# Kernel optimization log

Hardware: AMD Instinct MI355X
Metric: run time of the kernel (lower is better)

## Reference

```python
import jax, jax.numpy as jnp
import numpy as np

EDGE_TYPES = 5
D = 256      # input_dim == output_dim
HID = 128    # hard-coded hidden size of agg MLPs


def setup_inputs() -> dict:
    key = jax.random.key(0)
    ks = jax.random.split(key, 8)
    B, E, N = 4, 8000, 2000
    edge_distribution = jax.random.uniform(ks[0], (B, E, EDGE_TYPES), dtype=jnp.float32)
    H = jax.random.normal(ks[1], (B, E, N), dtype=jnp.float32)
    ori = jax.random.normal(ks[2], (B, N, D), dtype=jnp.float32)
    # Stacked per-edge-type MLP params: Linear(D->128), ReLU, Linear(128->D)
    W1 = jax.random.normal(ks[3], (EDGE_TYPES, D, HID), dtype=jnp.float32) * (1.0 / np.sqrt(D))
    b1 = jax.random.normal(ks[4], (EDGE_TYPES, HID), dtype=jnp.float32) * 0.01
    W2 = jax.random.normal(ks[5], (EDGE_TYPES, HID, D), dtype=jnp.float32) * (1.0 / np.sqrt(HID))
    b2 = jax.random.normal(ks[6], (EDGE_TYPES, D), dtype=jnp.float32) * 0.01
    return {"edge_distribution": edge_distribution, "H": H, "ori": ori,
            "W1": W1, "b1": b1, "W2": W2, "b2": b2}


def reference(edge_distribution, H, ori, W1, b1, W2, b2):
    # edges = H @ ori : [B, E, D]
    edges = jnp.matmul(H, ori)
    # Per-edge-type 2-layer MLP, vectorized over the type axis t
    h = jax.nn.relu(jnp.einsum('bed,tdh->tbeh', edges, W1) + b1[:, None, None, :])  # [T,B,E,HID]
    mlp_out = jnp.einsum('tbeh,thd->tbed', h, W2) + b2[:, None, None, :]            # [T,B,E,D]
    # Gated accumulate: sum_t edge_distribution[...,t] * mlp_out[t]
    edge_feature = jnp.einsum('bet,tbed->bed', edge_distribution, mlp_out)          # [B,E,D]
    # node_feature = concat(H^T @ edge_feature, ori)
    node_feature = jnp.concatenate(
        [jnp.matmul(jnp.swapaxes(H, 1, 2), edge_feature), ori], axis=-1)            # [B,N,2D]
    return node_feature
```

## Files before the change

### kernel.cpp

```cpp
#include <hip/hip_runtime.h>
#include <hip/hip_bf16.h>

typedef unsigned short u16;
typedef short bf16x8 __attribute__((ext_vector_type(8)));
typedef float f32x4 __attribute__((ext_vector_type(4)));
typedef unsigned short u16x8 __attribute__((ext_vector_type(8)));

#define GLL16(gp, lp) __builtin_amdgcn_global_load_lds( \
    (__attribute__((address_space(1))) const unsigned int*)(gp), \
    (__attribute__((address_space(3))) unsigned int*)(lp), 16, 0, 0)

static __device__ __forceinline__ u16 f2bf(float f){
  return __builtin_bit_cast(u16, __float2bfloat16(f));
}

__global__ void transpose_f32(const float* __restrict__ src, u16* __restrict__ dst,
                              int R, int C, int Rpad, long sB, long dB){
  __shared__ u16 tile[32][33];
  const int b = blockIdx.z;
  src += (long)b*sB; dst += (long)b*dB;
  const int r0 = blockIdx.x*32, c0 = blockIdx.y*32;
  const int j = threadIdx.x & 31, i0 = threadIdx.x >> 5;
  #pragma unroll
  for (int ii=0; ii<32; ii+=8){
    int r = r0+i0+ii, c = c0+j;
    u16 v = 0;
    if (r < R && c < C) v = f2bf(src[(long)r*C + c]);
    tile[i0+ii][j] = v;
  }
  __syncthreads();
  #pragma unroll
  for (int ii=0; ii<32; ii+=8){
    int c = c0+i0+ii, r = r0+j;
    if (c < C && r < Rpad) dst[(long)c*Rpad + r] = tile[j][i0+ii];
  }
}

__global__ __launch_bounds__(512,2) void g1_kernel(
    const float* __restrict__ Hm, const u16* __restrict__ oriT,
    u16* __restrict__ edges, u16* __restrict__ HT){
  __shared__ u16 As[2][128*32];
  __shared__ u16 Bs[2][256*32];
  __shared__ u16 At[2][32*136];
  const int b = blockIdx.y, bm = blockIdx.x*128;
  const int tid = threadIdx.x;
  const int w = tid>>6, quad = (tid&63)>>4, l16 = tid&15;
  const int wm = (w&1)*64, wn = (w>>1)*64;
  const float* Ab = Hm + (size_t)b*8000*2000 + (size_t)bm*2000;
  const u16*  Bb = oriT + (size_t)b*256*2048;
  u16* HTb = HT + (size_t)b*2048*8000;
  const bool edge_blk = (bm == 7936);

  float4 pa[2];
  auto loadA = [&](int kt, bool guard){
    const int k0 = kt*32;
    #pragma unroll
    for (int i=0;i<2;i++){
      int idx = i*512+tid, row = idx>>3, c4 = (idx&7)*4;
      if (!guard){
        pa[i] = *(const float4*)(Ab + (size_t)row*2000 + k0+c4);
      } else {
        bool ok = (bm+row < 8000) && (k0+c4 < 2000);
        pa[i] = ok ? *(const float4*)(Ab + (size_t)row*2000 + k0+c4) : make_float4(0.f,0.f,0.f,0.f);
      }
    }
  };
  auto storeA = [&](int kt){
    const int buf = kt&1;
    #pragma unroll
    for (int i=0;i<2;i++){
      int idx = i*512+tid, row = idx>>3, c4 = (idx&7)*4;
      ushort4 o; o.x=f2bf(pa[i].x); o.y=f2bf(pa[i].y); o.z=f2bf(pa[i].z); o.w=f2bf(pa[i].w);
      *(ushort4*)(&As[buf][idx*4]) = o;
      At[buf][(c4+0)*136 + (row ^ ((((c4+0)>>3)&3)<<3))] = o.x;
      At[buf][(c4+1)*136 + (row ^ ((((c4+1)>>3)&3)<<3))] = o.y;
      At[buf][(c4+2)*136 + (row ^ ((((c4+2)>>3)&3)<<3))] = o.z;
      At[buf][(c4+3)*136 + (row ^ ((((c4+3)>>3)&3)<<3))] = o.w;
    }
  };
  auto stageB = [&](int kt){
    const int buf = kt&1, k0 = kt*32;
    #pragma unroll
    for (int i=0;i<2;i++){
      int idx = i*512+tid;
      int row = idx>>2, c8 = (idx&3)*8;
      GLL16(Bb + (size_t)row*2048 + k0+c8, &Bs[buf][(i*512 + w*64)*8]);
    }
  };

  f32x4 acc[4][4];
  #pragma unroll
  for (int i=0;i<4;i++)
    #pragma unroll
    for (int j=0;j<4;j++) acc[i][j] = (f32x4){0.f,0.f,0.f,0.f};

  loadA(0, edge_blk); stageB(0);
  for (int kt=0; kt<64; kt++){
    storeA(kt);
    __syncthreads();
    if (kt+1 < 64){ loadA(kt+1, edge_blk || (kt+1 >= 62)); stageB(kt+1); }
    const int buf = kt&1, k0 = kt*32;
    {
      int kk = tid>>4, c = tid&15, m0 = c*8;
      if (bm + m0 < 8000){
        u16x8 v = *(const u16x8*)(&At[buf][kk*136 + (m0 ^ (((kk>>3)&3)<<3))]);
        *(u16x8*)(HTb + (size_t)(k0+kk)*8000 + bm + m0) = v;
      }
    }
    bf16x8 af[4], bf[4];
    #pragma unroll
    for (int mi=0;mi<4;mi++) af[mi] = *(const bf16x8*)(&As[buf][(wm+mi*16+l16)*32 + quad*8]);
    #pragma unroll
    for (int ni=0;ni<4;ni++) bf[ni] = *(const bf16x8*)(&Bs[buf][(wn+ni*16+l16)*32 + quad*8]);
    #pragma unroll
    for (int mi=0;mi<4;mi++)
      #pragma unroll
      for (int ni=0;ni<4;ni++)
        acc[mi][ni] = __builtin_amdgcn_mfma_f32_16x16x32_bf16(af[mi], bf[ni], acc[mi][ni], 0,0,0);
  }
  #pragma unroll
  for (int mi=0;mi<4;mi++){
    #pragma unroll
    for (int r=0;r<4;r++){
      int gm = bm + wm + mi*16 + quad*4 + r;
      if (gm >= 8000) continue;
      u16* dst = edges + ((size_t)b*8000 + gm)*256;
      #pragma unroll
      for (int ni=0;ni<4;ni++) dst[wn + ni*16 + l16] = f2bf(acc[mi][ni][r]);
    }
  }
}

__global__ __launch_bounds__(512,2) void mlp_kernel(
    const u16* __restrict__ edges, const u16* __restrict__ W1T, const u16* __restrict__ W2T,
    const float* __restrict__ b1, const float* __restrict__ b2,
    const float* __restrict__ edist, u16* __restrict__ EFt){
  __shared__ u16 Es[8*4096];
  __shared__ u16 Hs[4*4096];
  __shared__ u16 Bs[2][256*32];
  __shared__ float eds[640], b1s[640], b2s[1280];
  const int bm = blockIdx.x*128;
  const int tid = threadIdx.x;
  const int w = tid>>6, quad = (tid&63)>>4, l16 = tid&15;
  const int wm1 = (w&1)*64, wh1 = (w>>1)*32;
  const int wd2 = (w&3)*64, wm2 = (w>>2)*64;

  for (int i=tid;i<640;i+=512){ eds[i] = edist[(size_t)bm*5 + i]; b1s[i] = b1[i]; }
  for (int i=tid;i<1280;i+=512) b2s[i] = b2[i];

  const u16* Eb = edges + (size_t)bm*256;
  {
    int row = tid>>2, c8 = (tid&3)*8;
    #pragma unroll
    for (int kt=0;kt<8;kt++)
      GLL16(Eb + (size_t)row*256 + kt*32 + c8, &Es[kt*4096 + (w*64)*8]);
  }

  auto stage1 = [&](int t, int kt){
    const int buf = kt&1;
    int row = tid>>2, c8 = (tid&3)*8;
    GLL16(W1T + ((size_t)t*128 + row)*256 + kt*32 + c8, &Bs[buf][(w*64)*8]);
  };
  auto stage2 = [&](int t, int kk){
    const int buf = kk&1;
    #pragma unroll
    for (int i=0;i<2;i++){
      int idx = i*512+tid, row = idx>>2, c8 = (idx&3)*8;
      GLL16(W2T + ((size_t)t*256 + row)*128 + kk*32 + c8, &Bs[buf][(i*512 + w*64)*8]);
    }
  };

  f32x4 acc2[4][4];
  #pragma unroll
  for (int i=0;i<4;i++)
    #pragma unroll
    for (int j=0;j<4;j++) acc2[i][j] = (f32x4){0.f,0.f,0.f,0.f};

  stage1(0,0);
  for (int t=0;t<5;t++){
    f32x4 acc1[4][2];
    #pragma unroll
    for (int i=0;i<4;i++){ acc1[i][0] = (f32x4){0.f,0.f,0.f,0.f}; acc1[i][1] = (f32x4){0.f,0.f,0.f,0.f}; }
    for (int kt=0;kt<8;kt++){
      __syncthreads();
      if (kt<7) stage1(t,kt+1); else stage2(t,0);
      const int buf = kt&1;
      bf16x8 af[4], bfr[2];
      #pragma unroll
      for (int mi=0;mi<4;mi++) af[mi] = *(const bf16x8*)(&Es[kt*4096 + (wm1+mi*16+l16)*32 + quad*8]);
      #pragma unroll
      for (int ni=0;ni<2;ni++) bfr[ni] = *(const bf16x8*)(&Bs[buf][(wh1+ni*16+l16)*32 + quad*8]);
      #pragma unroll
      for (int mi=0;mi<4;mi++)
        #pragma unroll
        for (int ni=0;ni<2;ni++)
          acc1[mi][ni] = __builtin_amdgcn_mfma_f32_16x16x32_bf16(af[mi], bfr[ni], acc1[mi][ni], 0,0,0);
    }
    __syncthreads();
    #pragma unroll
    for (int mi=0;mi<4;mi++){
      #pragma unroll
      for (int r=0;r<4;r++){
        int lrow = wm1 + mi*16 + quad*4 + r;
        float s = eds[lrow*5 + t];
        #pragma unroll
        for (int ni=0;ni<2;ni++){
          int ch = wh1 + ni*16 + l16;
          float v = fmaxf(acc1[mi][ni][r] + b1s[t*128 + ch], 0.f) * s;
          Hs[(w>>1)*4096 + lrow*32 + (ni*16 + l16)] = f2bf(v);
        }
      }
    }
    for (int kk=0;kk<4;kk++){
      __syncthreads();
      if (kk<3) stage2(t,kk+1); else if (t<4) stage1(t+1,0);
      const int buf = kk&1;
      bf16x8 af2[4], bf2[4];
      #pragma unroll
      for (int mi=0;mi<4;mi++) af2[mi] = *(const bf16x8*)(&Bs[buf][(wd2+mi*16+l16)*32 + quad*8]);
      #pragma unroll
      for (int ni=0;ni<4;ni++) bf2[ni] = *(const bf16x8*)(&Hs[kk*4096 + (wm2+ni*16+l16)*32 + quad*8]);
      #pragma unroll
      for (int mi=0;mi<4;mi++)
        #pragma unroll
        for (int ni=0;ni<4;ni++)
          acc2[mi][ni] = __builtin_amdgcn_mfma_f32_16x16x32_bf16(af2[mi], bf2[ni], acc2[mi][ni], 0,0,0);
    }
  }
  #pragma unroll
  for (int mi=0;mi<4;mi++){
    #pragma unroll
    for (int r=0;r<4;r++){
      int d = wd2 + mi*16 + quad*4 + r;
      #pragma unroll
      for (int ni=0;ni<4;ni++){
        int mc = wm2 + ni*16 + l16;
        float bias = eds[mc*5+0]*b2s[d] + eds[mc*5+1]*b2s[256+d] + eds[mc*5+2]*b2s[512+d]
                   + eds[mc*5+3]*b2s[768+d] + eds[mc*5+4]*b2s[1024+d];
        int e = bm + mc;
        int bq = e / 8000;
        EFt[((size_t)bq*256 + d)*8000 + (e - bq*8000)] = f2bf(acc2[mi][ni][r] + bias);
      }
    }
  }
}

__global__ __launch_bounds__(512,2) void g3_kernel(
    const u16* __restrict__ HT, const u16* __restrict__ EFt, float* __restrict__ part){
  __shared__ u16 As[2][128*32];
  __shared__ u16 Bs[2][256*32];
  const int wg = ((int)blockIdx.x & 7)*32 + ((int)blockIdx.x >> 3);
  const int bm = (wg & 15)*128, ks = (wg>>4)&3, b = wg>>6;
  const int tid = threadIdx.x;
  const int w = tid>>6, quad = (tid&63)>>4, l16 = tid&15;
  const int wm = (w&1)*64, wn = (w>>1)*64;
  const u16* Ab = HT + (size_t)b*2048*8000 + (size_t)bm*8000;
  const u16* Bb = EFt + (size_t)b*256*8000;
  const int it0 = (250*ks)/4, it1 = (250*(ks+1))/4;

  auto stage = [&](int kt){
    const int buf = kt&1, k0 = kt*32;
    {
      int row = tid>>2, c8 = (tid&3)*8;
      GLL16(Ab + (size_t)row*8000 + k0+c8, &As[buf][(w*64)*8]);
    }
    #pragma unroll
    for (int i=0;i<2;i++){
      int idx = i*512+tid, row = idx>>2, c8 = (idx&3)*8;
      GLL16(Bb + (size_t)row*8000 + k0+c8, &Bs[buf][(i*512 + w*64)*8]);
    }
  };

  f32x4 acc[4][4];
  #pragma unroll
  for (int i=0;i<4;i++)
    #pragma unroll
    for (int j=0;j<4;j++) acc[i][j] = (f32x4){0.f,0.f,0.f,0.f};

  stage(it0);
  for (int kt=it0; kt<it1; kt++){
    __syncthreads();
    if (kt+1 < it1) stage(kt+1);
    const int buf = kt&1;
    bf16x8 af[4], bf[4];
    #pragma unroll
    for (int mi=0;mi<4;mi++) af[mi] = *(const bf16x8*)(&As[buf][(wm+mi*16+l16)*32 + quad*8]);
    #pragma unroll
    for (int ni=0;ni<4;ni++) bf[ni] = *(const bf16x8*)(&Bs[buf][(wn+ni*16+l16)*32 + quad*8]);
    #pragma unroll
    for (int mi=0;mi<4;mi++)
      #pragma unroll
      for (int ni=0;ni<4;ni++)
        acc[mi][ni] = __builtin_amdgcn_mfma_f32_16x16x32_bf16(af[mi], bf[ni], acc[mi][ni], 0,0,0);
  }
  float* dst0 = part + ((size_t)(b*4 + ks)*2048)*256;
  #pragma unroll
  for (int mi=0;mi<4;mi++){
    #pragma unroll
    for (int r=0;r<4;r++){
      int gm = bm + wm + mi*16 + quad*4 + r;
      float* dst = dst0 + (size_t)gm*256;
      #pragma unroll
      for (int ni=0;ni<4;ni++) dst[wn + ni*16 + l16] = acc[mi][ni][r];
    }
  }
}

__global__ void assemble_kernel(const float* __restrict__ part, const float* __restrict__ ori,
                                float* __restrict__ out){
  const int b = blockIdx.y;
  int u = blockIdx.x*256 + threadIdx.x;
  int n = u>>6, c4 = (u&63)*4;
  f32x4 s = (f32x4){0.f,0.f,0.f,0.f};
  #pragma unroll
  for (int ks=0; ks<4; ks++)
    s += *(const f32x4*)(part + ((size_t)(b*4+ks)*2048 + n)*256 + c4);
  float* dst = out + ((size_t)(b*2000+n))*512;
  *(f32x4*)(dst + c4) = s;
  *(f32x4*)(dst + 256 + c4) = *(const f32x4*)(ori + ((size_t)(b*2000+n))*256 + c4);
}

extern "C" void kernel_launch(void* const* d_in, const int* in_sizes, int n_in,
                              void* d_out, int out_size, void* d_ws, size_t ws_size,
                              hipStream_t stream) {
  const float* ed  = (const float*)d_in[0];
  const float* Hm  = (const float*)d_in[1];
  const float* ori = (const float*)d_in[2];
  const float* W1  = (const float*)d_in[3];
  const float* b1  = (const float*)d_in[4];
  const float* W2  = (const float*)d_in[5];
  const float* b2  = (const float*)d_in[6];
  float* out = (float*)d_out;
  char* ws = (char*)d_ws;

  u16* HT    = (u16*)(ws);
  u16* oriT  = (u16*)(ws + 131072000);
  u16* W1T   = (u16*)(ws + 135266304);
  u16* W2T   = (u16*)(ws + 135593984);
  u16* edges = (u16*)(ws + 135921664);
  u16* EFt   = (u16*)(ws + 152305664);
  float* part = (float*)(ws + 168689664);

  hipLaunchKernelGGL(transpose_f32, dim3(64,8,4), dim3(256), 0, stream,
                     ori, oriT, 2000, 256, 2048, 512000L, 524288L);
  hipLaunchKernelGGL(transpose_f32, dim3(8,4,5), dim3(256), 0, stream,
                     W1, W1T, 256, 128, 256, 32768L, 32768L);
  hipLaunchKernelGGL(transpose_f32, dim3(4,8,5), dim3(256), 0, stream,
                     W2, W2T, 128, 256, 128, 32768L, 32768L);

  hipLaunchKernelGGL(g1_kernel, dim3(63,4), dim3(512), 0, stream, Hm, oriT, edges, HT);
  hipLaunchKernelGGL(mlp_kernel, dim3(250), dim3(512), 0, stream,
                     edges, W1T, W2T, b1, b2, ed, EFt);
  hipLaunchKernelGGL(g3_kernel, dim3(256), dim3(512), 0, stream, HT, EFt, part);
  hipLaunchKernelGGL(assemble_kernel, dim3(500,4), dim3(256), 0, stream, part, ori, out);

  (void)in_sizes; (void)n_in; (void)ws_size;
}
```

Baseline: 542.0 us.

## Halve M-tile to 64 rows with 256-thread blocks across GEMM and MLP kernels

Shrinks the row tile of the three main kernels from 128 to 64 with 4 waves per block, doubling the grid sizes (125x4, 500, 512 blocks). This puts more blocks on the CUs and, since 8000 is a multiple of 64, removes the boundary guards for the last tile. The MLP kernel now streams the edge tile through a double buffer per k-step instead of holding the whole 128x256 tile in LDS, which lowers LDS use but reloads the edge rows for each of the five edge types. Smaller tiles also mean more global traffic per FLOP for the shared B operands.

```diff
diff --git a/kernel.cpp b/kernel.cpp
--- a/kernel.cpp
+++ b/kernel.cpp
@@ -36,31 +36,30 @@
   }
 }
 
-__global__ __launch_bounds__(512,2) void g1_kernel(
+__global__ __launch_bounds__(256,2) void g1_kernel(
     const float* __restrict__ Hm, const u16* __restrict__ oriT,
     u16* __restrict__ edges, u16* __restrict__ HT){
-  __shared__ u16 As[2][128*32];
+  __shared__ u16 As[2][64*32];
   __shared__ u16 Bs[2][256*32];
-  __shared__ u16 At[2][32*136];
-  const int b = blockIdx.y, bm = blockIdx.x*128;
+  __shared__ u16 At[2][32*72];
+  const int b = blockIdx.y, bm = blockIdx.x*64;
   const int tid = threadIdx.x;
   const int w = tid>>6, quad = (tid&63)>>4, l16 = tid&15;
-  const int wm = (w&1)*64, wn = (w>>1)*64;
+  const int wn = w*64;
   const float* Ab = Hm + (size_t)b*8000*2000 + (size_t)bm*2000;
   const u16*  Bb = oriT + (size_t)b*256*2048;
   u16* HTb = HT + (size_t)b*2048*8000;
-  const bool edge_blk = (bm == 7936);
 
   float4 pa[2];
   auto loadA = [&](int kt, bool guard){
     const int k0 = kt*32;
     #pragma unroll
     for (int i=0;i<2;i++){
-      int idx = i*512+tid, row = idx>>3, c4 = (idx&7)*4;
+      int idx = i*256+tid, row = idx>>3, c4 = (idx&7)*4;
       if (!guard){
         pa[i] = *(const float4*)(Ab + (size_t)row*2000 + k0+c4);
       } else {
-        bool ok = (bm+row < 8000) && (k0+c4 < 2000);
+        bool ok = (k0+c4 < 2000);
         pa[i] = ok ? *(const float4*)(Ab + (size_t)row*2000 + k0+c4) : make_float4(0.f,0.f,0.f,0.f);
       }
     }
@@ -69,22 +68,22 @@
     const int buf = kt&1;
     #pragma unroll
     for (int i=0;i<2;i++){
-      int idx = i*512+tid, row = idx>>3, c4 = (idx&7)*4;
+      int idx = i*256+tid, row = idx>>3, c4 = (idx&7)*4;
       ushort4 o; o.x=f2bf(pa[i].x); o.y=f2bf(pa[i].y); o.z=f2bf(pa[i].z); o.w=f2bf(pa[i].w);
       *(ushort4*)(&As[buf][idx*4]) = o;
-      At[buf][(c4+0)*136 + (row ^ ((((c4+0)>>3)&3)<<3))] = o.x;
-      At[buf][(c4+1)*136 + (row ^ ((((c4+1)>>3)&3)<<3))] = o.y;
-      At[buf][(c4+2)*136 + (row ^ ((((c4+2)>>3)&3)<<3))] = o.z;
-      At[buf][(c4+3)*136 + (row ^ ((((c4+3)>>3)&3)<<3))] = o.w;
+      At[buf][(c4+0)*72 + (row ^ ((((c4+0)>>3)&3)<<3))] = o.x;
+      At[buf][(c4+1)*72 + (row ^ ((((c4+1)>>3)&3)<<3))] = o.y;
+      At[buf][(c4+2)*72 + (row ^ ((((c4+2)>>3)&3)<<3))] = o.z;
+      At[buf][(c4+3)*72 + (row ^ ((((c4+3)>>3)&3)<<3))] = o.w;
     }
   };
   auto stageB = [&](int kt){
     const int buf = kt&1, k0 = kt*32;
     #pragma unroll
-    for (int i=0;i<2;i++){
-      int idx = i*512+tid;
+    for (int i=0;i<4;i++){
+      int idx = i*256+tid;
       int row = idx>>2, c8 = (idx&3)*8;
-      GLL16(Bb + (size_t)row*2048 + k0+c8, &Bs[buf][(i*512 + w*64)*8]);
+      GLL16(Bb + (size_t)row*2048 + k0+c8, &Bs[buf][(i*256 + w*64)*8]);
     }
   };
 
@@ -94,22 +93,20 @@
     #pragma unroll
     for (int j=0;j<4;j++) acc[i][j] = (f32x4){0.f,0.f,0.f,0.f};
 
-  loadA(0, edge_blk); stageB(0);
+  loadA(0, false); stageB(0);
   for (int kt=0; kt<64; kt++){
     storeA(kt);
     __syncthreads();
-    if (kt+1 < 64){ loadA(kt+1, edge_blk || (kt+1 >= 62)); stageB(kt+1); }
+    if (kt+1 < 64){ loadA(kt+1, kt+1 >= 62); stageB(kt+1); }
     const int buf = kt&1, k0 = kt*32;
     {
-      int kk = tid>>4, c = tid&15, m0 = c*8;
-      if (bm + m0 < 8000){
-        u16x8 v = *(const u16x8*)(&At[buf][kk*136 + (m0 ^ (((kk>>3)&3)<<3))]);
-        *(u16x8*)(HTb + (size_t)(k0+kk)*8000 + bm + m0) = v;
-      }
+      int kk = tid>>3, m0 = (tid&7)*8;
+      u16x8 v = *(const u16x8*)(&At[buf][kk*72 + (m0 ^ (((kk>>3)&3)<<3))]);
+      *(u16x8*)(HTb + (size_t)(k0+kk)*8000 + bm + m0) = v;
     }
     bf16x8 af[4], bf[4];
     #pragma unroll
-    for (int mi=0;mi<4;mi++) af[mi] = *(const bf16x8*)(&As[buf][(wm+mi*16+l16)*32 + quad*8]);
+    for (int mi=0;mi<4;mi++) af[mi] = *(const bf16x8*)(&As[buf][(mi*16+l16)*32 + quad*8]);
     #pragma unroll
     for (int ni=0;ni<4;ni++) bf[ni] = *(const bf16x8*)(&Bs[buf][(wn+ni*16+l16)*32 + quad*8]);
     #pragma unroll
@@ -122,8 +119,7 @@
   for (int mi=0;mi<4;mi++){
     #pragma unroll
     for (int r=0;r<4;r++){
-      int gm = bm + wm + mi*16 + quad*4 + r;
-      if (gm >= 8000) continue;
+      int gm = bm + mi*16 + quad*4 + r;
       u16* dst = edges + ((size_t)b*8000 + gm)*256;
       #pragma unroll
       for (int ni=0;ni<4;ni++) dst[wn + ni*16 + l16] = f2bf(acc[mi][ni][r]);
@@ -131,42 +127,45 @@
   }
 }
 
-__global__ __launch_bounds__(512,2) void mlp_kernel(
+__global__ __launch_bounds__(256,2) void mlp_kernel(
     const u16* __restrict__ edges, const u16* __restrict__ W1T, const u16* __restrict__ W2T,
     const float* __restrict__ b1, const float* __restrict__ b2,
     const float* __restrict__ edist, u16* __restrict__ EFt){
-  __shared__ u16 Es[8*4096];
-  __shared__ u16 Hs[4*4096];
+  __shared__ u16 As[2][64*32];
+  __shared__ u16 Hs[4*2048];
   __shared__ u16 Bs[2][256*32];
-  __shared__ float eds[640], b1s[640], b2s[1280];
-  const int bm = blockIdx.x*128;
+  __shared__ float eds[320], b1s[640], b2s[1280];
+  const int bm = blockIdx.x*64;
   const int tid = threadIdx.x;
   const int w = tid>>6, quad = (tid&63)>>4, l16 = tid&15;
-  const int wm1 = (w&1)*64, wh1 = (w>>1)*32;
-  const int wd2 = (w&3)*64, wm2 = (w>>2)*64;
-
-  for (int i=tid;i<640;i+=512){ eds[i] = edist[(size_t)bm*5 + i]; b1s[i] = b1[i]; }
-  for (int i=tid;i<1280;i+=512) b2s[i] = b2[i];
+  const int wh1 = w*32;
+  const int wd2 = w*64;
+
+  for (int i=tid;i<320;i+=256) eds[i] = edist[(size_t)bm*5 + i];
+  for (int i=tid;i<640;i+=256) b1s[i] = b1[i];
+  for (int i=tid;i<1280;i+=256) b2s[i] = b2[i];
 
   const u16* Eb = edges + (size_t)bm*256;
-  {
-    int row = tid>>2, c8 = (tid&3)*8;
-    #pragma unroll
-    for (int kt=0;kt<8;kt++)
-      GLL16(Eb + (size_t)row*256 + kt*32 + c8, &Es[kt*4096 + (w*64)*8]);
-  }
-
-  auto stage1 = [&](int t, int kt){
+
+  auto stageA = [&](int kt){
     const int buf = kt&1;
     int row = tid>>2, c8 = (tid&3)*8;
-    GLL16(W1T + ((size_t)t*128 + row)*256 + kt*32 + c8, &Bs[buf][(w*64)*8]);
-  };
-  auto stage2 = [&](int t, int kk){
+    GLL16(Eb + (size_t)row*256 + kt*32 + c8, &As[buf][(w*64)*8]);
+  };
+  auto stageW1 = [&](int t, int kt){
+    const int buf = kt&1;
+    #pragma unroll
+    for (int i=0;i<2;i++){
+      int idx = i*256+tid, row = idx>>2, c8 = (idx&3)*8;
+      GLL16(W1T + ((size_t)t*128 + row)*256 + kt*32 + c8, &Bs[buf][(i*256 + w*64)*8]);
+    }
+  };
+  auto stageW2 = [&](int t, int kk){
     const int buf = kk&1;
     #pragma unroll
-    for (int i=0;i<2;i++){
-      int idx = i*512+tid, row = idx>>2, c8 = (idx&3)*8;
-      GLL16(W2T + ((size_t)t*256 + row)*128 + kk*32 + c8, &Bs[buf][(i*512 + w*64)*8]);
+    for (int i=0;i<4;i++){
+      int idx = i*256+tid, row = idx>>2, c8 = (idx&3)*8;
+      GLL16(W2T + ((size_t)t*256 + row)*128 + kk*32 + c8, &Bs[buf][(i*256 + w*64)*8]);
     }
   };
 
@@ -176,18 +175,18 @@
     #pragma unroll
     for (int j=0;j<4;j++) acc2[i][j] = (f32x4){0.f,0.f,0.f,0.f};
 
-  stage1(0,0);
+  stageA(0); stageW1(0,0);
   for (int t=0;t<5;t++){
     f32x4 acc1[4][2];
     #pragma unroll
     for (int i=0;i<4;i++){ acc1[i][0] = (f32x4){0.f,0.f,0.f,0.f}; acc1[i][1] = (f32x4){0.f,0.f,0.f,0.f}; }
     for (int kt=0;kt<8;kt++){
       __syncthreads();
-      if (kt<7) stage1(t,kt+1); else stage2(t,0);
+      if (kt<7){ stageA(kt+1); stageW1(t,kt+1); } else stageW2(t,0);
       const int buf = kt&1;
       bf16x8 af[4], bfr[2];
       #pragma unroll
-      for (int mi=0;mi<4;mi++) af[mi] = *(const bf16x8*)(&Es[kt*4096 + (wm1+mi*16+l16)*32 + quad*8]);
+      for (int mi=0;mi<4;mi++) af[mi] = *(const bf16x8*)(&As[buf][(mi*16+l16)*32 + quad*8]);
       #pragma unroll
       for (int ni=0;ni<2;ni++) bfr[ni] = *(const bf16x8*)(&Bs[buf][(wh1+ni*16+l16)*32 + quad*8]);
       #pragma unroll
@@ -201,25 +200,26 @@
     for (int mi=0;mi<4;mi++){
       #pragma unroll
       for (int r=0;r<4;r++){
-        int lrow = wm1 + mi*16 + quad*4 + r;
+        int lrow = mi*16 + quad*4 + r;
         float s = eds[lrow*5 + t];
         #pragma unroll
         for (int ni=0;ni<2;ni++){
           int ch = wh1 + ni*16 + l16;
           float v = fmaxf(acc1[mi][ni][r] + b1s[t*128 + ch], 0.f) * s;
-          Hs[(w>>1)*4096 + lrow*32 + (ni*16 + l16)] = f2bf(v);
+          Hs[(ch>>5)*2048 + lrow*32 + (ch&31)] = f2bf(v);
         }
       }
     }
     for (int kk=0;kk<4;kk++){
       __syncthreads();
-      if (kk<3) stage2(t,kk+1); else if (t<4) stage1(t+1,0);
+      if (kk<3) stageW2(t,kk+1);
+      else if (t<4){ stageA(0); stageW1(t+1,0); }
       const int buf = kk&1;
       bf16x8 af2[4], bf2[4];
       #pragma unroll
       for (int mi=0;mi<4;mi++) af2[mi] = *(const bf16x8*)(&Bs[buf][(wd2+mi*16+l16)*32 + quad*8]);
       #pragma unroll
-      for (int ni=0;ni<4;ni++) bf2[ni] = *(const bf16x8*)(&Hs[kk*4096 + (wm2+ni*16+l16)*32 + quad*8]);
+      for (int ni=0;ni<4;ni++) bf2[ni] = *(const bf16x8*)(&Hs[kk*2048 + (ni*16+l16)*32 + quad*8]);
       #pragma unroll
       for (int mi=0;mi<4;mi++)
         #pragma unroll
@@ -234,7 +234,7 @@
       int d = wd2 + mi*16 + quad*4 + r;
       #pragma unroll
       for (int ni=0;ni<4;ni++){
-        int mc = wm2 + ni*16 + l16;
+        int mc = ni*16 + l16;
         float bias = eds[mc*5+0]*b2s[d] + eds[mc*5+1]*b2s[256+d] + eds[mc*5+2]*b2s[512+d]
                    + eds[mc*5+3]*b2s[768+d] + eds[mc*5+4]*b2s[1024+d];
         int e = bm + mc;
@@ -245,15 +245,15 @@
   }
 }
 
-__global__ __launch_bounds__(512,2) void g3_kernel(
+__global__ __launch_bounds__(256,2) void g3_kernel(
     const u16* __restrict__ HT, const u16* __restrict__ EFt, float* __restrict__ part){
-  __shared__ u16 As[2][128*32];
+  __shared__ u16 As[2][64*32];
   __shared__ u16 Bs[2][256*32];
-  const int wg = ((int)blockIdx.x & 7)*32 + ((int)blockIdx.x >> 3);
-  const int bm = (wg & 15)*128, ks = (wg>>4)&3, b = wg>>6;
+  const int wg = ((int)blockIdx.x & 7)*64 + ((int)blockIdx.x >> 3);
+  const int bm = (wg & 31)*64, ks = (wg>>5)&3, b = wg>>7;
   const int tid = threadIdx.x;
   const int w = tid>>6, quad = (tid&63)>>4, l16 = tid&15;
-  const int wm = (w&1)*64, wn = (w>>1)*64;
+  const int wn = w*64;
   const u16* Ab = HT + (size_t)b*2048*8000 + (size_t)bm*8000;
   const u16* Bb = EFt + (size_t)b*256*8000;
   const int it0 = (250*ks)/4, it1 = (250*(ks+1))/4;
@@ -265,9 +265,9 @@
       GLL16(Ab + (size_t)row*8000 + k0+c8, &As[buf][(w*64)*8]);
     }
     #pragma unroll
-    for (int i=0;i<2;i++){
-      int idx = i*512+tid, row = idx>>2, c8 = (idx&3)*8;
-      GLL16(Bb + (size_t)row*8000 + k0+c8, &Bs[buf][(i*512 + w*64)*8]);
+    for (int i=0;i<4;i++){
+      int idx = i*256+tid, row = idx>>2, c8 = (idx&3)*8;
+      GLL16(Bb + (size_t)row*8000 + k0+c8, &Bs[buf][(i*256 + w*64)*8]);
     }
   };
 
@@ -284,7 +284,7 @@
     const int buf = kt&1;
     bf16x8 af[4], bf[4];
     #pragma unroll
-    for (int mi=0;mi<4;mi++) af[mi] = *(const bf16x8*)(&As[buf][(wm+mi*16+l16)*32 + quad*8]);
+    for (int mi=0;mi<4;mi++) af[mi] = *(const bf16x8*)(&As[buf][(mi*16+l16)*32 + quad*8]);
     #pragma unroll
     for (int ni=0;ni<4;ni++) bf[ni] = *(const bf16x8*)(&Bs[buf][(wn+ni*16+l16)*32 + quad*8]);
     #pragma unroll
@@ -298,7 +298,7 @@
   for (int mi=0;mi<4;mi++){
     #pragma unroll
     for (int r=0;r<4;r++){
-      int gm = bm + wm + mi*16 + quad*4 + r;
+      int gm = bm + mi*16 + quad*4 + r;
       float* dst = dst0 + (size_t)gm*256;
       #pragma unroll
       for (int ni=0;ni<4;ni++) dst[wn + ni*16 + l16] = acc[mi][ni][r];
@@ -348,10 +348,10 @@
   hipLaunchKernelGGL(transpose_f32, dim3(4,8,5), dim3(256), 0, stream,
                      W2, W2T, 128, 256, 128, 32768L, 32768L);
 
-  hipLaunchKernelGGL(g1_kernel, dim3(63,4), dim3(512), 0, stream, Hm, oriT, edges, HT);
-  hipLaunchKernelGGL(mlp_kernel, dim3(250), dim3(512), 0, stream,
+  hipLaunchKernelGGL(g1_kernel, dim3(125,4), dim3(256), 0, stream, Hm, oriT, edges, HT);
+  hipLaunchKernelGGL(mlp_kernel, dim3(500), dim3(256), 0, stream,
                      edges, W1T, W2T, b1, b2, ed, EFt);
-  hipLaunchKernelGGL(g3_kernel, dim3(256), dim3(512), 0, stream, HT, EFt, part);
+  hipLaunchKernelGGL(g3_kernel, dim3(512), dim3(256), 0, stream, HT, EFt, part);
   hipLaunchKernelGGL(assemble_kernel, dim3(500,4), dim3(256), 0, stream, part, ori, out);
 
   (void)in_sizes; (void)n_in; (void)ws_size;
```

After: 554.7 us. +2.4%, slower.

## Fuse the H@ori GEMM with the per-type MLP in one kernel

Applied to the files above, without the earlier changes.

Merges the first GEMM (edges = H@ori) and the gated per-edge-type MLP into a single kernel. The GEMM accumulator tile is written straight into shared memory as the MLP's input, so the bf16 edges tensor no longer goes to global memory and one kernel launch is removed. Shared memory grows to about 138 KB per block, which likely limits occupancy to one block per CU despite launch_bounds(512,2). The fused grid of 252 blocks also runs the MLP with partial-tile waste in the tail block of each batch.

```diff
diff --git a/kernel.cpp b/kernel.cpp
--- a/kernel.cpp
+++ b/kernel.cpp
@@ -36,12 +36,21 @@
   }
 }
 
-__global__ __launch_bounds__(512,2) void g1_kernel(
+__global__ __launch_bounds__(512,2) void g1mlp_kernel(
     const float* __restrict__ Hm, const u16* __restrict__ oriT,
-    u16* __restrict__ edges, u16* __restrict__ HT){
-  __shared__ u16 As[2][128*32];
-  __shared__ u16 Bs[2][256*32];
-  __shared__ u16 At[2][32*136];
+    const u16* __restrict__ W1T, const u16* __restrict__ W2T,
+    const float* __restrict__ b1, const float* __restrict__ b2,
+    const float* __restrict__ edist, u16* __restrict__ HT, u16* __restrict__ EFt){
+  __shared__ __align__(16) char smem[141312];
+  u16*   Bs  = (u16*)(smem);
+  float* eds = (float*)(smem + 32768);
+  float* b1s = (float*)(smem + 35328);
+  float* b2s = (float*)(smem + 37888);
+  u16*   As  = (u16*)(smem + 43008);
+  u16*   At  = (u16*)(smem + 59392);
+  u16*   Es  = (u16*)(smem + 43008);
+  u16*   Hs  = (u16*)(smem + 108544);
+
   const int b = blockIdx.y, bm = blockIdx.x*128;
   const int tid = threadIdx.x;
   const int w = tid>>6, quad = (tid&63)>>4, l16 = tid&15;
@@ -51,6 +60,13 @@
   u16* HTb = HT + (size_t)b*2048*8000;
   const bool edge_blk = (bm == 7936);
 
+  for (int i=tid;i<640;i+=512){
+    int e = bm + i/5;
+    eds[i] = (e < 8000) ? edist[((size_t)b*8000 + bm)*5 + i] : 0.f;
+  }
+  for (int i=tid;i<640;i+=512)  b1s[i] = b1[i];
+  for (int i=tid;i<1280;i+=512) b2s[i] = b2[i];
+
   float4 pa[2];
   auto loadA = [&](int kt, bool guard){
     const int k0 = kt*32;
@@ -71,11 +87,11 @@
     for (int i=0;i<2;i++){
       int idx = i*512+tid, row = idx>>3, c4 = (idx&7)*4;
       ushort4 o; o.x=f2bf(pa[i].x); o.y=f2bf(pa[i].y); o.z=f2bf(pa[i].z); o.w=f2bf(pa[i].w);
-      *(ushort4*)(&As[buf][idx*4]) = o;
-      At[buf][(c4+0)*136 + (row ^ ((((c4+0)>>3)&3)<<3))] = o.x;
-      At[buf][(c4+1)*136 + (row ^ ((((c4+1)>>3)&3)<<3))] = o.y;
-      At[buf][(c4+2)*136 + (row ^ ((((c4+2)>>3)&3)<<3))] = o.z;
-      At[buf][(c4+3)*136 + (row ^ ((((c4+3)>>3)&3)<<3))] = o.w;
+      *(ushort4*)(&As[buf*4096 + idx*4]) = o;
+      At[buf*4352 + (c4+0)*136 + (row ^ ((((c4+0)>>3)&3)<<3))] = o.x;
+      At[buf*4352 + (c4+1)*136 + (row ^ ((((c4+1)>>3)&3)<<3))] = o.y;
+      At[buf*4352 + (c4+2)*136 + (row ^ ((((c4+2)>>3)&3)<<3))] = o.z;
+      At[buf*4352 + (c4+3)*136 + (row ^ ((((c4+3)>>3)&3)<<3))] = o.w;
     }
   };
   auto stageB = [&](int kt){
@@ -84,7 +100,7 @@
     for (int i=0;i<2;i++){
       int idx = i*512+tid;
       int row = idx>>2, c8 = (idx&3)*8;
-      GLL16(Bb + (size_t)row*2048 + k0+c8, &Bs[buf][(i*512 + w*64)*8]);
+      GLL16(Bb + (size_t)row*2048 + k0+c8, &Bs[buf*8192 + (i*512 + w*64)*8]);
     }
   };
 
@@ -103,70 +119,55 @@
     {
       int kk = tid>>4, c = tid&15, m0 = c*8;
       if (bm + m0 < 8000){
-        u16x8 v = *(const u16x8*)(&At[buf][kk*136 + (m0 ^ (((kk>>3)&3)<<3))]);
+        u16x8 v = *(const u16x8*)(&At[buf*4352 + kk*136 + (m0 ^ (((kk>>3)&3)<<3))]);
         *(u16x8*)(HTb + (size_t)(k0+kk)*8000 + bm + m0) = v;
       }
     }
     bf16x8 af[4], bf[4];
     #pragma unroll
-    for (int mi=0;mi<4;mi++) af[mi] = *(const bf16x8*)(&As[buf][(wm+mi*16+l16)*32 + quad*8]);
-    #pragma unroll
-    for (int ni=0;ni<4;ni++) bf[ni] = *(const bf16x8*)(&Bs[buf][(wn+ni*16+l16)*32 + quad*8]);
+    for (int mi=0;mi<4;mi++) af[mi] = *(const bf16x8*)(&As[buf*4096 + (wm+mi*16+l16)*32 + quad*8]);
+    #pragma unroll
+    for (int ni=0;ni<4;ni++) bf[ni] = *(const bf16x8*)(&Bs[buf*8192 + (wn+ni*16+l16)*32 + quad*8]);
     #pragma unroll
     for (int mi=0;mi<4;mi++)
       #pragma unroll
       for (int ni=0;ni<4;ni++)
         acc[mi][ni] = __builtin_amdgcn_mfma_f32_16x16x32_bf16(af[mi], bf[ni], acc[mi][ni], 0,0,0);
   }
-  #pragma unroll
-  for (int mi=0;mi<4;mi++){
-    #pragma unroll
-    for (int r=0;r<4;r++){
-      int gm = bm + wm + mi*16 + quad*4 + r;
-      if (gm >= 8000) continue;
-      u16* dst = edges + ((size_t)b*8000 + gm)*256;
-      #pragma unroll
-      for (int ni=0;ni<4;ni++) dst[wn + ni*16 + l16] = f2bf(acc[mi][ni][r]);
-    }
-  }
-}
-
-__global__ __launch_bounds__(512,2) void mlp_kernel(
-    const u16* __restrict__ edges, const u16* __restrict__ W1T, const u16* __restrict__ W2T,
-    const float* __restrict__ b1, const float* __restrict__ b2,
-    const float* __restrict__ edist, u16* __restrict__ EFt){
-  __shared__ u16 Es[8*4096];
-  __shared__ u16 Hs[4*4096];
-  __shared__ u16 Bs[2][256*32];
-  __shared__ float eds[640], b1s[640], b2s[1280];
-  const int bm = blockIdx.x*128;
-  const int tid = threadIdx.x;
-  const int w = tid>>6, quad = (tid&63)>>4, l16 = tid&15;
-  const int wm1 = (w&1)*64, wh1 = (w>>1)*32;
-  const int wd2 = (w&3)*64, wm2 = (w>>2)*64;
-
-  for (int i=tid;i<640;i+=512){ eds[i] = edist[(size_t)bm*5 + i]; b1s[i] = b1[i]; }
-  for (int i=tid;i<1280;i+=512) b2s[i] = b2[i];
-
-  const u16* Eb = edges + (size_t)bm*256;
+
+  __syncthreads();
   {
     int row = tid>>2, c8 = (tid&3)*8;
-    #pragma unroll
-    for (int kt=0;kt<8;kt++)
-      GLL16(Eb + (size_t)row*256 + kt*32 + c8, &Es[kt*4096 + (w*64)*8]);
-  }
-
-  auto stage1 = [&](int t, int kt){
+    GLL16(W1T + (size_t)row*256 + c8, &Bs[0*8192 + (w*64)*8]);
+  }
+  #pragma unroll
+  for (int mi=0;mi<4;mi++){
+    #pragma unroll
+    for (int r=0;r<4;r++){
+      int m = wm + mi*16 + quad*4 + r;
+      #pragma unroll
+      for (int ni=0;ni<4;ni++){
+        int d = wn + ni*16 + l16;
+        Es[(d>>5)*4096 + m*32 + (d&31)] = f2bf(acc[mi][ni][r]);
+      }
+    }
+  }
+  __syncthreads();
+
+  const int wm1 = (w&1)*64, wh1 = ((w>>1)&3)*32;
+  const int wd2 = (w&3)*64, wm2 = (w>>2)*64;
+
+  auto stageW1 = [&](int t, int kt){
     const int buf = kt&1;
     int row = tid>>2, c8 = (tid&3)*8;
-    GLL16(W1T + ((size_t)t*128 + row)*256 + kt*32 + c8, &Bs[buf][(w*64)*8]);
-  };
-  auto stage2 = [&](int t, int kk){
+    GLL16(W1T + ((size_t)t*128 + row)*256 + kt*32 + c8, &Bs[buf*8192 + (w*64)*8]);
+  };
+  auto stageW2 = [&](int t, int kk){
     const int buf = kk&1;
     #pragma unroll
     for (int i=0;i<2;i++){
       int idx = i*512+tid, row = idx>>2, c8 = (idx&3)*8;
-      GLL16(W2T + ((size_t)t*256 + row)*128 + kk*32 + c8, &Bs[buf][(i*512 + w*64)*8]);
+      GLL16(W2T + ((size_t)t*256 + row)*128 + kk*32 + c8, &Bs[buf*8192 + (i*512 + w*64)*8]);
     }
   };
 
@@ -176,27 +177,25 @@
     #pragma unroll
     for (int j=0;j<4;j++) acc2[i][j] = (f32x4){0.f,0.f,0.f,0.f};
 
-  stage1(0,0);
   for (int t=0;t<5;t++){
     f32x4 acc1[4][2];
     #pragma unroll
     for (int i=0;i<4;i++){ acc1[i][0] = (f32x4){0.f,0.f,0.f,0.f}; acc1[i][1] = (f32x4){0.f,0.f,0.f,0.f}; }
     for (int kt=0;kt<8;kt++){
-      __syncthreads();
-      if (kt<7) stage1(t,kt+1); else stage2(t,0);
+      if (kt<7) stageW1(t,kt+1); else stageW2(t,0);
       const int buf = kt&1;
       bf16x8 af[4], bfr[2];
       #pragma unroll
       for (int mi=0;mi<4;mi++) af[mi] = *(const bf16x8*)(&Es[kt*4096 + (wm1+mi*16+l16)*32 + quad*8]);
       #pragma unroll
-      for (int ni=0;ni<2;ni++) bfr[ni] = *(const bf16x8*)(&Bs[buf][(wh1+ni*16+l16)*32 + quad*8]);
+      for (int ni=0;ni<2;ni++) bfr[ni] = *(const bf16x8*)(&Bs[buf*8192 + (wh1+ni*16+l16)*32 + quad*8]);
       #pragma unroll
       for (int mi=0;mi<4;mi++)
         #pragma unroll
         for (int ni=0;ni<2;ni++)
           acc1[mi][ni] = __builtin_amdgcn_mfma_f32_16x16x32_bf16(af[mi], bfr[ni], acc1[mi][ni], 0,0,0);
-    }
-    __syncthreads();
+      __syncthreads();
+    }
     #pragma unroll
     for (int mi=0;mi<4;mi++){
       #pragma unroll
@@ -207,17 +206,17 @@
         for (int ni=0;ni<2;ni++){
           int ch = wh1 + ni*16 + l16;
           float v = fmaxf(acc1[mi][ni][r] + b1s[t*128 + ch], 0.f) * s;
-          Hs[(w>>1)*4096 + lrow*32 + (ni*16 + l16)] = f2bf(v);
+          Hs[(ch>>5)*4096 + lrow*32 + (ch&31)] = f2bf(v);
         }
       }
     }
+    __syncthreads();
     for (int kk=0;kk<4;kk++){
-      __syncthreads();
-      if (kk<3) stage2(t,kk+1); else if (t<4) stage1(t+1,0);
+      if (kk<3) stageW2(t,kk+1); else if (t<4) stageW1(t+1,0);
       const int buf = kk&1;
       bf16x8 af2[4], bf2[4];
       #pragma unroll
-      for (int mi=0;mi<4;mi++) af2[mi] = *(const bf16x8*)(&Bs[buf][(wd2+mi*16+l16)*32 + quad*8]);
+      for (int mi=0;mi<4;mi++) af2[mi] = *(const bf16x8*)(&Bs[buf*8192 + (wd2+mi*16+l16)*32 + quad*8]);
       #pragma unroll
       for (int ni=0;ni<4;ni++) bf2[ni] = *(const bf16x8*)(&Hs[kk*4096 + (wm2+ni*16+l16)*32 + quad*8]);
       #pragma unroll
@@ -225,6 +224,7 @@
         #pragma unroll
         for (int ni=0;ni<4;ni++)
           acc2[mi][ni] = __builtin_amdgcn_mfma_f32_16x16x32_bf16(af2[mi], bf2[ni], acc2[mi][ni], 0,0,0);
+      __syncthreads();
     }
   }
   #pragma unroll
@@ -235,11 +235,12 @@
       #pragma unroll
       for (int ni=0;ni<4;ni++){
         int mc = wm2 + ni*16 + l16;
-        float bias = eds[mc*5+0]*b2s[d] + eds[mc*5+1]*b2s[256+d] + eds[mc*5+2]*b2s[512+d]
-                   + eds[mc*5+3]*b2s[768+d] + eds[mc*5+4]*b2s[1024+d];
         int e = bm + mc;
-        int bq = e / 8000;
-        EFt[((size_t)bq*256 + d)*8000 + (e - bq*8000)] = f2bf(acc2[mi][ni][r] + bias);
+        if (e < 8000){
+          float bias = eds[mc*5+0]*b2s[d] + eds[mc*5+1]*b2s[256+d] + eds[mc*5+2]*b2s[512+d]
+                     + eds[mc*5+3]*b2s[768+d] + eds[mc*5+4]*b2s[1024+d];
+          EFt[((size_t)b*256 + d)*8000 + e] = f2bf(acc2[mi][ni][r] + bias);
+        }
       }
     }
   }
@@ -337,7 +338,6 @@
   u16* oriT  = (u16*)(ws + 131072000);
   u16* W1T   = (u16*)(ws + 135266304);
   u16* W2T   = (u16*)(ws + 135593984);
-  u16* edges = (u16*)(ws + 135921664);
   u16* EFt   = (u16*)(ws + 152305664);
   float* part = (float*)(ws + 168689664);
 
@@ -348,9 +348,8 @@
   hipLaunchKernelGGL(transpose_f32, dim3(4,8,5), dim3(256), 0, stream,
                      W2, W2T, 128, 256, 128, 32768L, 32768L);
 
-  hipLaunchKernelGGL(g1_kernel, dim3(63,4), dim3(512), 0, stream, Hm, oriT, edges, HT);
-  hipLaunchKernelGGL(mlp_kernel, dim3(250), dim3(512), 0, stream,
-                     edges, W1T, W2T, b1, b2, ed, EFt);
+  hipLaunchKernelGGL(g1mlp_kernel, dim3(63,4), dim3(512), 0, stream,
+                     Hm, oriT, W1T, W2T, b1, b2, ed, HT, EFt);
   hipLaunchKernelGGL(g3_kernel, dim3(256), dim3(512), 0, stream, HT, EFt, part);
   hipLaunchKernelGGL(assemble_kernel, dim3(500,4), dim3(256), 0, stream, part, ori, out);
 
```

After: 529.2 us. 1.02x faster.
